# Optimization experiments

Hardware: AMD Instinct MI355X
Metric: run time of the kernel (lower is better)

## Reference

```python
import jax, jax.numpy as jnp
import numpy as np

N_NODES = 50000
N_EDGES = 600000
N_GRAPHS = 100
IN_DIM, HID, OUT = 128, 128, 64
K = 2  # DGL TAGConv default hop count


def setup_inputs() -> dict:
    key = jax.random.key(0)
    ks = jax.random.split(key, 8)
    x = jax.random.normal(ks[0], (N_NODES, IN_DIM), dtype=jnp.float32)
    src = jax.random.randint(ks[1], (N_EDGES,), 0, N_NODES)
    dst = jax.random.randint(ks[2], (N_EDGES,), 0, N_NODES)
    graph_id = jnp.sort(jax.random.randint(ks[3], (N_NODES,), 0, N_GRAPHS))
    # TAGConv lin: Linear(in_feats*(K+1), out_feats), stored as (in*(K+1), out)
    W1 = jax.random.normal(ks[4], (IN_DIM * (K + 1), HID), dtype=jnp.float32) / np.sqrt(IN_DIM * (K + 1))
    b1 = jnp.zeros((HID,), dtype=jnp.float32)
    W2 = jax.random.normal(ks[5], (HID * (K + 1), OUT), dtype=jnp.float32) / np.sqrt(HID * (K + 1))
    b2 = jnp.zeros((OUT,), dtype=jnp.float32)
    return {"x": x, "W1": W1, "b1": b1, "W2": W2, "b2": b2,
            "src": src, "dst": dst, "graph_id": graph_id}


def _tagconv(h, src, dst, norm, W, b):
    """DGL TAGConv: relu(concat_k (D^-1/2 A D^-1/2)^k h @ W + b), k=0..K."""
    feats = [h]
    cur = h
    for _ in range(K):
        cur = cur * norm[:, None]
        cur = jax.ops.segment_sum(cur[src], dst, num_segments=N_NODES)
        cur = cur * norm[:, None]
        feats.append(cur)
    out = jnp.concatenate(feats, axis=-1) @ W + b
    return jax.nn.relu(out)


def reference(x, W1, b1, W2, b2, src, dst, graph_id):
    # symmetric norm from in-degrees (clamped to 1), as in DGL TAGConv
    deg = jax.ops.segment_sum(jnp.ones_like(dst, dtype=x.dtype), dst, num_segments=N_NODES)
    norm = jnp.clip(deg, 1.0, None) ** -0.5
    h = _tagconv(x, src, dst, norm, W1, b1)
    h = _tagconv(h, src, dst, norm, W2, b2)
    # MaxPooling readout: per-graph max over nodes
    return jax.ops.segment_max(h, graph_id, num_segments=N_GRAPHS)
```

## Files before the change

kernel.cpp:

```cpp
#include <hip/hip_runtime.h>
#include <hip/hip_bf16.h>

#define N_NODES 50000
#define N_EDGES 600000
#define N_GRAPHS 100
#define M_PAD 50176

typedef __bf16 bf16_t;
typedef __attribute__((ext_vector_type(8))) __bf16 bf16x8;
typedef __attribute__((ext_vector_type(4))) __bf16 bf16x4;
typedef __attribute__((ext_vector_type(2))) __bf16 bf16x2;
typedef __attribute__((ext_vector_type(4))) float f32x4;

__global__ void degk(const int* __restrict__ dst, int* __restrict__ deg, int n) {
    int i = blockIdx.x * 256 + threadIdx.x;
    if (i < n) atomicAdd(&deg[dst[i]], 1);
}

__global__ __launch_bounds__(1024) void scan1(const int* __restrict__ deg,
                                              int* __restrict__ row_off,
                                              int* __restrict__ partial,
                                              float* __restrict__ norm, int n) {
    __shared__ int buf[1024];
    int i = blockIdx.x * 1024 + threadIdx.x;
    int v = (i < n) ? deg[i] : 0;
    buf[threadIdx.x] = v;
    __syncthreads();
    for (int off = 1; off < 1024; off <<= 1) {
        int t = (threadIdx.x >= off) ? buf[threadIdx.x - off] : 0;
        __syncthreads();
        buf[threadIdx.x] += t;
        __syncthreads();
    }
    if (i < n) {
        row_off[i + 1] = buf[threadIdx.x];
        float d = fmaxf((float)v, 1.0f);
        norm[i] = 1.0f / sqrtf(d);
    }
    if (threadIdx.x == 1023) partial[blockIdx.x] = buf[1023];
}

__global__ __launch_bounds__(256) void scan3(int* __restrict__ row_off,
                                             const int* __restrict__ partial, int n) {
    int i = blockIdx.x * 256 + threadIdx.x;
    int c = (blockIdx.x * 256) >> 10;
    __shared__ int pre;
    if (threadIdx.x < 64) {
        int v = (threadIdx.x < c) ? partial[threadIdx.x] : 0;
        for (int off = 32; off; off >>= 1) v += __shfl_down(v, off, 64);
        if (threadIdx.x == 0) pre = v;
    }
    __syncthreads();
    if (i == 0) row_off[0] = 0;
    if (i < n) row_off[i + 1] += pre;
}

#define NPRE 6250
#define NSC  ((N_EDGES + 255) / 256)
#define NPW  ((384 * 192 + 255) / 256)
__global__ __launch_bounds__(256) void midk(const float* __restrict__ x,
                                            const float* __restrict__ norm,
                                            bf16_t* __restrict__ xb, bf16_t* __restrict__ xs,
                                            const int* __restrict__ src, const int* __restrict__ dst,
                                            const int* __restrict__ row_off, int* __restrict__ cursor,
                                            int* __restrict__ csr_src,
                                            const float* __restrict__ W1, bf16_t* __restrict__ Wp1,
                                            const float* __restrict__ W2, bf16_t* __restrict__ Wp2) {
    int b = blockIdx.x;
    if (b < NPRE) {
        int i = b * 256 + threadIdx.x;
        int node = i >> 5, c4 = i & 31;
        float4 v = *(const float4*)(x + (size_t)node * 128 + c4 * 4);
        float nd = norm[node];
        bf16x4 ob, os;
        ob[0] = (bf16_t)v.x; ob[1] = (bf16_t)v.y; ob[2] = (bf16_t)v.z; ob[3] = (bf16_t)v.w;
        os[0] = (bf16_t)(v.x * nd); os[1] = (bf16_t)(v.y * nd);
        os[2] = (bf16_t)(v.z * nd); os[3] = (bf16_t)(v.w * nd);
        *(bf16x4*)(xb + (size_t)node * 128 + c4 * 4) = ob;
        *(bf16x4*)(xs + (size_t)node * 128 + c4 * 4) = os;
    } else if (b < NPRE + NSC) {
        int e = (b - NPRE) * 256 + threadIdx.x;
        if (e >= N_EDGES) return;
        int d = dst[e];
        int pos = atomicAdd(&cursor[d], 1);
        csr_src[row_off[d] + pos] = src[e];
    } else {
        int i = (b - NPRE - NSC) * 256 + threadIdx.x;
        const float* W; bf16_t* Wp; int N; int idx;
        if (i < 384 * 128)                 { W = W1; Wp = Wp1; N = 128; idx = i; }
        else if (i < 384 * 128 + 384 * 64) { W = W2; Wp = Wp2; N = 64;  idx = i - 384 * 128; }
        else return;
        int k = idx / N, n = idx - k * N;
        int kt = k >> 5, q = (k >> 3) & 3, j = k & 7;
        int nt = n >> 4, ln = n & 15;
        int lane = q * 16 + ln;
        Wp[(((size_t)kt * (N >> 4) + nt) * 64 + lane) * 8 + j] = (bf16_t)W[idx];
    }
}

template <bool SCALED>
__global__ __launch_bounds__(256) void spmm_bf16(const bf16_t* __restrict__ in,
                                                 bf16_t* __restrict__ out_c,
                                                 bf16_t* __restrict__ out_s,
                                                 const float* __restrict__ norm,
                                                 const int* __restrict__ row_off,
                                                 const int* __restrict__ csr_src, int n) {
    int tid = threadIdx.x;
    int sub = tid >> 4;
    int l   = tid & 15;
    int node = blockIdx.x * 16 + sub;
    if (node >= n) return;
    int e0 = row_off[node], e1 = row_off[node + 1];
    const bf16_t* col = in + l * 8;
    float acc[8] = {};
    int e = e0;
    for (; e + 8 <= e1; e += 8) {
        int s0 = csr_src[e + 0];
        int s1 = csr_src[e + 1];
        int s2 = csr_src[e + 2];
        int s3 = csr_src[e + 3];
        int s4 = csr_src[e + 4];
        int s5 = csr_src[e + 5];
        int s6 = csr_src[e + 6];
        int s7 = csr_src[e + 7];
        bf16x8 v0 = *(const bf16x8*)(col + (size_t)s0 * 128);
        bf16x8 v1 = *(const bf16x8*)(col + (size_t)s1 * 128);
        bf16x8 v2 = *(const bf16x8*)(col + (size_t)s2 * 128);
        bf16x8 v3 = *(const bf16x8*)(col + (size_t)s3 * 128);
        bf16x8 v4 = *(const bf16x8*)(col + (size_t)s4 * 128);
        bf16x8 v5 = *(const bf16x8*)(col + (size_t)s5 * 128);
        bf16x8 v6 = *(const bf16x8*)(col + (size_t)s6 * 128);
        bf16x8 v7 = *(const bf16x8*)(col + (size_t)s7 * 128);
#pragma unroll
        for (int j = 0; j < 8; j++)
            acc[j] += (((float)v0[j] + (float)v1[j]) + ((float)v2[j] + (float)v3[j]))
                    + (((float)v4[j] + (float)v5[j]) + ((float)v6[j] + (float)v7[j]));
    }
    if (e + 4 <= e1) {
        int s0 = csr_src[e + 0];
        int s1 = csr_src[e + 1];
        int s2 = csr_src[e + 2];
        int s3 = csr_src[e + 3];
        bf16x8 v0 = *(const bf16x8*)(col + (size_t)s0 * 128);
        bf16x8 v1 = *(const bf16x8*)(col + (size_t)s1 * 128);
        bf16x8 v2 = *(const bf16x8*)(col + (size_t)s2 * 128);
        bf16x8 v3 = *(const bf16x8*)(col + (size_t)s3 * 128);
#pragma unroll
        for (int j = 0; j < 8; j++)
            acc[j] += ((float)v0[j] + (float)v1[j]) + ((float)v2[j] + (float)v3[j]);
        e += 4;
    }
    for (; e < e1; e++) {
        int s = csr_src[e];
        bf16x8 v = *(const bf16x8*)(col + (size_t)s * 128);
#pragma unroll
        for (int j = 0; j < 8; j++) acc[j] += (float)v[j];
    }
    float nd = norm[node];
    bf16x8 oc, os;
#pragma unroll
    for (int j = 0; j < 8; j++) {
        float c = acc[j] * nd;
        oc[j] = (bf16_t)c;
        os[j] = (bf16_t)(c * nd);
    }
    *(bf16x8*)(out_c + (size_t)node * 128 + l * 8) = oc;
    if (SCALED) *(bf16x8*)(out_s + (size_t)node * 128 + l * 8) = os;
}

template <int NT, bool LAYER1>
__global__ __launch_bounds__(256) void gemm_mfma(const bf16_t* __restrict__ f0,
                                                 const bf16_t* __restrict__ f1,
                                                 const bf16_t* __restrict__ f2,
                                                 const bf16_t* __restrict__ Wp,
                                                 const float* __restrict__ bias,
                                                 const float* __restrict__ norm,
                                                 bf16_t* __restrict__ out_b,
                                                 bf16_t* __restrict__ out_s,
                                                 float* __restrict__ out_f, int M) {
    int wave = threadIdx.x >> 6;
    int lane = threadIdx.x & 63;
    int q = lane >> 4, ln = lane & 15;
    int row0 = blockIdx.x * 128 + wave * 32;

    f32x4 acc[2][NT] = {};
    const bf16_t* feats[3] = {f0, f1, f2};
    const bf16x8* Wf = (const bf16x8*)Wp;

#pragma unroll
    for (int kc = 0; kc < 12; kc++) {
        const bf16_t* A = feats[kc >> 2] + (size_t)(kc & 3) * 32 + q * 8;
        bf16x8 a0 = *(const bf16x8*)(A + (size_t)(row0 + ln) * 128);
        bf16x8 a1 = *(const bf16x8*)(A + (size_t)(row0 + 16 + ln) * 128);
        const bf16x8* Bp = Wf + (size_t)kc * NT * 64 + lane;
#pragma unroll
        for (int nt = 0; nt < NT; nt++) {
            bf16x8 b = Bp[nt * 64];
            acc[0][nt] = __builtin_amdgcn_mfma_f32_16x16x32_bf16(a0, b, acc[0][nt], 0, 0, 0);
            acc[1][nt] = __builtin_amdgcn_mfma_f32_16x16x32_bf16(a1, b, acc[1][nt], 0, 0, 0);
        }
    }

    float bv[NT];
#pragma unroll
    for (int nt = 0; nt < NT; nt++) bv[nt] = bias[nt * 16 + ln];

#pragma unroll
    for (int mt = 0; mt < 2; mt++) {
#pragma unroll
        for (int r = 0; r < 4; r++) {
            int row = row0 + mt * 16 + q * 4 + r;
            if (row >= M) continue;
            float nd = LAYER1 ? norm[row] : 0.f;
#pragma unroll
            for (int nt = 0; nt < NT; nt++) {
                int col = nt * 16 + ln;
                float val = fmaxf(acc[mt][nt][r] + bv[nt], 0.f);
                if (LAYER1) {
                    out_b[(size_t)row * 128 + col] = (bf16_t)val;
                    out_s[(size_t)row * 128 + col] = (bf16_t)(val * nd);
                } else {
                    out_f[(size_t)row * 64 + col] = val;
                }
            }
        }
    }
}

__global__ __launch_bounds__(256) void maxpool2(const float* __restrict__ hF,
                                                const int* __restrict__ gid,
                                                unsigned int* __restrict__ out, int n) {
    int wave = threadIdx.x >> 6;
    int lane = threadIdx.x & 63;
    int n0 = blockIdx.x * 256 + wave * 64;
    if (n0 >= n) return;
    int n1 = min(n0 + 64, n);
    int cur = gid[n0];
    float m = 0.f;
    int i = n0;
    for (; i + 4 <= n1; i += 4) {
        int g0 = gid[i + 0], g1 = gid[i + 1], g2 = gid[i + 2], g3 = gid[i + 3];
        float v0 = hF[(size_t)(i + 0) * 64 + lane];
        float v1 = hF[(size_t)(i + 1) * 64 + lane];
        float v2 = hF[(size_t)(i + 2) * 64 + lane];
        float v3 = hF[(size_t)(i + 3) * 64 + lane];
        if (g0 != cur) { atomicMax(&out[cur * 64 + lane], __float_as_uint(m)); cur = g0; m = v0; } else m = fmaxf(m, v0);
        if (g1 != cur) { atomicMax(&out[cur * 64 + lane], __float_as_uint(m)); cur = g1; m = v1; } else m = fmaxf(m, v1);
        if (g2 != cur) { atomicMax(&out[cur * 64 + lane], __float_as_uint(m)); cur = g2; m = v2; } else m = fmaxf(m, v2);
        if (g3 != cur) { atomicMax(&out[cur * 64 + lane], __float_as_uint(m)); cur = g3; m = v3; } else m = fmaxf(m, v3);
    }
    for (; i < n1; i++) {
        int g = gid[i];
        float v = hF[(size_t)i * 64 + lane];
        if (g != cur) { atomicMax(&out[cur * 64 + lane], __float_as_uint(m)); cur = g; m = v; }
        else m = fmaxf(m, v);
    }
    atomicMax(&out[cur * 64 + lane], __float_as_uint(m));
}

extern "C" void kernel_launch(void* const* d_in, const int* in_sizes, int n_in,
                              void* d_out, int out_size, void* d_ws, size_t ws_size,
                              hipStream_t stream) {
    const float* x  = (const float*)d_in[0];
    const float* W1 = (const float*)d_in[1];
    const float* b1 = (const float*)d_in[2];
    const float* W2 = (const float*)d_in[3];
    const float* b2 = (const float*)d_in[4];
    const int* src  = (const int*)d_in[5];
    const int* dst  = (const int*)d_in[6];
    const int* gid  = (const int*)d_in[7];
    float* out = (float*)d_out;

    char* ws = (char*)d_ws;
    size_t off = 0;
    auto take = [&](size_t bytes) {
        void* p = ws + off;
        off = (off + bytes + 255) & ~(size_t)255;
        return p;
    };
    int* deg     = (int*)take((size_t)N_NODES * 4);
    int* cursor  = (int*)take((size_t)N_NODES * 4);
    size_t zero_bytes = off;
    float* norm  = (float*)take((size_t)N_NODES * 4);
    int* row_off = (int*)take((size_t)(N_NODES + 1) * 4);
    int* partial = (int*)take(64 * 4);
    int* csr_src = (int*)take((size_t)N_EDGES * 4);
    bf16_t* Wp1  = (bf16_t*)take((size_t)384 * 128 * 2);
    bf16_t* Wp2  = (bf16_t*)take((size_t)384 * 64 * 2);
    bf16_t* B0 = (bf16_t*)take((size_t)M_PAD * 128 * 2);
    bf16_t* B1 = (bf16_t*)take((size_t)M_PAD * 128 * 2);
    bf16_t* B2 = (bf16_t*)take((size_t)M_PAD * 128 * 2);
    bf16_t* B3 = (bf16_t*)take((size_t)M_PAD * 128 * 2);
    bf16_t* B4 = (bf16_t*)take((size_t)M_PAD * 128 * 2);
    bf16_t* B5 = (bf16_t*)take((size_t)M_PAD * 128 * 2);
    (void)ws_size; (void)in_sizes; (void)n_in; (void)out_size;

    hipMemsetAsync(d_ws, 0, zero_bytes, stream);
    hipMemsetAsync(d_out, 0, (size_t)N_GRAPHS * 64 * 4, stream);

    degk<<<(N_EDGES + 255) / 256, 256, 0, stream>>>(dst, deg, N_EDGES);
    int nchunks = (N_NODES + 1023) / 1024;
    scan1<<<nchunks, 1024, 0, stream>>>(deg, row_off, partial, norm, N_NODES);
    scan3<<<(N_NODES + 255) / 256, 256, 0, stream>>>(row_off, partial, N_NODES);
    midk<<<NPRE + NSC + NPW, 256, 0, stream>>>(x, norm, B0, B1, src, dst, row_off, cursor,
                                               csr_src, W1, Wp1, W2, Wp2);

    int spmm_grid = (N_NODES + 15) / 16;
    int gemm_grid = M_PAD / 128;

    spmm_bf16<true><<<spmm_grid, 256, 0, stream>>>(B1, B2, B4, norm, row_off, csr_src, N_NODES);
    spmm_bf16<false><<<spmm_grid, 256, 0, stream>>>(B4, B3, nullptr, norm, row_off, csr_src, N_NODES);
    gemm_mfma<8, true><<<gemm_grid, 256, 0, stream>>>(B0, B2, B3, Wp1, b1, norm, B5, B1, nullptr, N_NODES);
    spmm_bf16<true><<<spmm_grid, 256, 0, stream>>>(B1, B2, B4, norm, row_off, csr_src, N_NODES);
    spmm_bf16<false><<<spmm_grid, 256, 0, stream>>>(B4, B3, nullptr, norm, row_off, csr_src, N_NODES);
    gemm_mfma<4, false><<<gemm_grid, 256, 0, stream>>>(B5, B2, B3, Wp2, b2, nullptr, nullptr, nullptr, (float*)B0, N_NODES);
    maxpool2<<<(N_NODES + 255) / 256, 256, 0, stream>>>((const float*)B0, gid, (unsigned int*)out, N_NODES);
}
```

Baseline: 310.2 us.

## Tile feature matrices into column slices mapped to XCDs for SpMM L2 locality

Feature buffers are stored as four 32-column slices, each laid out node-major. The SpMM grid is remapped so each pair of XCDs (by blockIdx & 7) gathers only one slice, shrinking each XCD's working set so it fits better in its private L2. Each node is now handled by 4 lanes instead of 16, so a wave covers 16 nodes. The CSR build also reuses the per-edge rank from the degree atomics instead of a second atomic cursor pass. The cost is an extra rank buffer and the assumption that the hardware dispatches blocks round-robin across XCDs.

```diff
diff --git a/kernel.cpp b/kernel.cpp
--- a/kernel.cpp
+++ b/kernel.cpp
@@ -5,6 +5,7 @@
 #define N_EDGES 600000
 #define N_GRAPHS 100
 #define M_PAD 50176
+#define TSLICE ((size_t)M_PAD * 32)
 
 typedef __bf16 bf16_t;
 typedef __attribute__((ext_vector_type(8))) __bf16 bf16x8;
@@ -12,9 +13,10 @@
 typedef __attribute__((ext_vector_type(2))) __bf16 bf16x2;
 typedef __attribute__((ext_vector_type(4))) float f32x4;
 
-__global__ void degk(const int* __restrict__ dst, int* __restrict__ deg, int n) {
+__global__ void degk(const int* __restrict__ dst, int* __restrict__ deg,
+                     int* __restrict__ rank, int n) {
     int i = blockIdx.x * 256 + threadIdx.x;
-    if (i < n) atomicAdd(&deg[dst[i]], 1);
+    if (i < n) rank[i] = atomicAdd(&deg[dst[i]], 1);
 }
 
 __global__ __launch_bounds__(1024) void scan1(const int* __restrict__ deg,
@@ -62,7 +64,8 @@
                                             const float* __restrict__ norm,
                                             bf16_t* __restrict__ xb, bf16_t* __restrict__ xs,
                                             const int* __restrict__ src, const int* __restrict__ dst,
-                                            const int* __restrict__ row_off, int* __restrict__ cursor,
+                                            const int* __restrict__ row_off,
+                                            const int* __restrict__ rank,
                                             int* __restrict__ csr_src,
                                             const float* __restrict__ W1, bf16_t* __restrict__ Wp1,
                                             const float* __restrict__ W2, bf16_t* __restrict__ Wp2) {
@@ -76,14 +79,14 @@
         ob[0] = (bf16_t)v.x; ob[1] = (bf16_t)v.y; ob[2] = (bf16_t)v.z; ob[3] = (bf16_t)v.w;
         os[0] = (bf16_t)(v.x * nd); os[1] = (bf16_t)(v.y * nd);
         os[2] = (bf16_t)(v.z * nd); os[3] = (bf16_t)(v.w * nd);
-        *(bf16x4*)(xb + (size_t)node * 128 + c4 * 4) = ob;
-        *(bf16x4*)(xs + (size_t)node * 128 + c4 * 4) = os;
+        size_t t = (size_t)(c4 >> 3) * TSLICE + (size_t)node * 32 + (c4 & 7) * 4;
+        *(bf16x4*)(xb + t) = ob;
+        *(bf16x4*)(xs + t) = os;
     } else if (b < NPRE + NSC) {
         int e = (b - NPRE) * 256 + threadIdx.x;
         if (e >= N_EDGES) return;
         int d = dst[e];
-        int pos = atomicAdd(&cursor[d], 1);
-        csr_src[row_off[d] + pos] = src[e];
+        csr_src[row_off[d] + rank[e]] = src[e];
     } else {
         int i = (b - NPRE - NSC) * 256 + threadIdx.x;
         const float* W; bf16_t* Wp; int N; int idx;
@@ -99,19 +102,22 @@
 }
 
 template <bool SCALED>
-__global__ __launch_bounds__(256) void spmm_bf16(const bf16_t* __restrict__ in,
-                                                 bf16_t* __restrict__ out_c,
-                                                 bf16_t* __restrict__ out_s,
-                                                 const float* __restrict__ norm,
-                                                 const int* __restrict__ row_off,
-                                                 const int* __restrict__ csr_src, int n) {
-    int tid = threadIdx.x;
-    int sub = tid >> 4;
-    int l   = tid & 15;
-    int node = blockIdx.x * 16 + sub;
+__global__ __launch_bounds__(256) void spmm_xcd(const bf16_t* __restrict__ in,
+                                                bf16_t* __restrict__ out_c,
+                                                bf16_t* __restrict__ out_s,
+                                                const float* __restrict__ norm,
+                                                const int* __restrict__ row_off,
+                                                const int* __restrict__ csr_src, int n) {
+    int bid  = blockIdx.x;
+    int xcd  = bid & 7;
+    int tile = xcd >> 1;
+    int sub  = bid >> 3;
+    int grp  = threadIdx.x >> 2;
+    int l    = threadIdx.x & 3;
+    int node = (sub * 2 + (xcd & 1)) * 64 + grp;
     if (node >= n) return;
     int e0 = row_off[node], e1 = row_off[node + 1];
-    const bf16_t* col = in + l * 8;
+    const bf16_t* base = in + (size_t)tile * TSLICE + l * 8;
     float acc[8] = {};
     int e = e0;
     for (; e + 8 <= e1; e += 8) {
@@ -123,14 +129,14 @@
         int s5 = csr_src[e + 5];
         int s6 = csr_src[e + 6];
         int s7 = csr_src[e + 7];
-        bf16x8 v0 = *(const bf16x8*)(col + (size_t)s0 * 128);
-        bf16x8 v1 = *(const bf16x8*)(col + (size_t)s1 * 128);
-        bf16x8 v2 = *(const bf16x8*)(col + (size_t)s2 * 128);
-        bf16x8 v3 = *(const bf16x8*)(col + (size_t)s3 * 128);
-        bf16x8 v4 = *(const bf16x8*)(col + (size_t)s4 * 128);
-        bf16x8 v5 = *(const bf16x8*)(col + (size_t)s5 * 128);
-        bf16x8 v6 = *(const bf16x8*)(col + (size_t)s6 * 128);
-        bf16x8 v7 = *(const bf16x8*)(col + (size_t)s7 * 128);
+        bf16x8 v0 = *(const bf16x8*)(base + (size_t)s0 * 32);
+        bf16x8 v1 = *(const bf16x8*)(base + (size_t)s1 * 32);
+        bf16x8 v2 = *(const bf16x8*)(base + (size_t)s2 * 32);
+        bf16x8 v3 = *(const bf16x8*)(base + (size_t)s3 * 32);
+        bf16x8 v4 = *(const bf16x8*)(base + (size_t)s4 * 32);
+        bf16x8 v5 = *(const bf16x8*)(base + (size_t)s5 * 32);
+        bf16x8 v6 = *(const bf16x8*)(base + (size_t)s6 * 32);
+        bf16x8 v7 = *(const bf16x8*)(base + (size_t)s7 * 32);
 #pragma unroll
         for (int j = 0; j < 8; j++)
             acc[j] += (((float)v0[j] + (float)v1[j]) + ((float)v2[j] + (float)v3[j]))
@@ -141,10 +147,10 @@
         int s1 = csr_src[e + 1];
         int s2 = csr_src[e + 2];
         int s3 = csr_src[e + 3];
-        bf16x8 v0 = *(const bf16x8*)(col + (size_t)s0 * 128);
-        bf16x8 v1 = *(const bf16x8*)(col + (size_t)s1 * 128);
-        bf16x8 v2 = *(const bf16x8*)(col + (size_t)s2 * 128);
-        bf16x8 v3 = *(const bf16x8*)(col + (size_t)s3 * 128);
+        bf16x8 v0 = *(const bf16x8*)(base + (size_t)s0 * 32);
+        bf16x8 v1 = *(const bf16x8*)(base + (size_t)s1 * 32);
+        bf16x8 v2 = *(const bf16x8*)(base + (size_t)s2 * 32);
+        bf16x8 v3 = *(const bf16x8*)(base + (size_t)s3 * 32);
 #pragma unroll
         for (int j = 0; j < 8; j++)
             acc[j] += ((float)v0[j] + (float)v1[j]) + ((float)v2[j] + (float)v3[j]);
@@ -152,7 +158,7 @@
     }
     for (; e < e1; e++) {
         int s = csr_src[e];
-        bf16x8 v = *(const bf16x8*)(col + (size_t)s * 128);
+        bf16x8 v = *(const bf16x8*)(base + (size_t)s * 32);
 #pragma unroll
         for (int j = 0; j < 8; j++) acc[j] += (float)v[j];
     }
@@ -164,8 +170,9 @@
         oc[j] = (bf16_t)c;
         os[j] = (bf16_t)(c * nd);
     }
-    *(bf16x8*)(out_c + (size_t)node * 128 + l * 8) = oc;
-    if (SCALED) *(bf16x8*)(out_s + (size_t)node * 128 + l * 8) = os;
+    size_t t = (size_t)tile * TSLICE + (size_t)node * 32 + l * 8;
+    *(bf16x8*)(out_c + t) = oc;
+    if (SCALED) *(bf16x8*)(out_s + t) = os;
 }
 
 template <int NT, bool LAYER1>
@@ -189,9 +196,9 @@
 
 #pragma unroll
     for (int kc = 0; kc < 12; kc++) {
-        const bf16_t* A = feats[kc >> 2] + (size_t)(kc & 3) * 32 + q * 8;
-        bf16x8 a0 = *(const bf16x8*)(A + (size_t)(row0 + ln) * 128);
-        bf16x8 a1 = *(const bf16x8*)(A + (size_t)(row0 + 16 + ln) * 128);
+        const bf16_t* A = feats[kc >> 2] + (size_t)(kc & 3) * TSLICE + q * 8;
+        bf16x8 a0 = *(const bf16x8*)(A + (size_t)(row0 + ln) * 32);
+        bf16x8 a1 = *(const bf16x8*)(A + (size_t)(row0 + 16 + ln) * 32);
         const bf16x8* Bp = Wf + (size_t)kc * NT * 64 + lane;
 #pragma unroll
         for (int nt = 0; nt < NT; nt++) {
@@ -214,13 +221,13 @@
             float nd = LAYER1 ? norm[row] : 0.f;
 #pragma unroll
             for (int nt = 0; nt < NT; nt++) {
-                int col = nt * 16 + ln;
                 float val = fmaxf(acc[mt][nt][r] + bv[nt], 0.f);
                 if (LAYER1) {
-                    out_b[(size_t)row * 128 + col] = (bf16_t)val;
-                    out_s[(size_t)row * 128 + col] = (bf16_t)(val * nd);
+                    size_t t = (size_t)(nt >> 1) * TSLICE + (size_t)row * 32 + (nt & 1) * 16 + ln;
+                    out_b[t] = (bf16_t)val;
+                    out_s[t] = (bf16_t)(val * nd);
                 } else {
-                    out_f[(size_t)row * 64 + col] = val;
+                    out_f[(size_t)row * 64 + nt * 16 + ln] = val;
                 }
             }
         }
@@ -279,11 +286,11 @@
         return p;
     };
     int* deg     = (int*)take((size_t)N_NODES * 4);
-    int* cursor  = (int*)take((size_t)N_NODES * 4);
     size_t zero_bytes = off;
     float* norm  = (float*)take((size_t)N_NODES * 4);
     int* row_off = (int*)take((size_t)(N_NODES + 1) * 4);
     int* partial = (int*)take(64 * 4);
+    int* rank    = (int*)take((size_t)N_EDGES * 4);
     int* csr_src = (int*)take((size_t)N_EDGES * 4);
     bf16_t* Wp1  = (bf16_t*)take((size_t)384 * 128 * 2);
     bf16_t* Wp2  = (bf16_t*)take((size_t)384 * 64 * 2);
@@ -298,21 +305,21 @@
     hipMemsetAsync(d_ws, 0, zero_bytes, stream);
     hipMemsetAsync(d_out, 0, (size_t)N_GRAPHS * 64 * 4, stream);
 
-    degk<<<(N_EDGES + 255) / 256, 256, 0, stream>>>(dst, deg, N_EDGES);
+    degk<<<(N_EDGES + 255) / 256, 256, 0, stream>>>(dst, deg, rank, N_EDGES);
     int nchunks = (N_NODES + 1023) / 1024;
     scan1<<<nchunks, 1024, 0, stream>>>(deg, row_off, partial, norm, N_NODES);
     scan3<<<(N_NODES + 255) / 256, 256, 0, stream>>>(row_off, partial, N_NODES);
-    midk<<<NPRE + NSC + NPW, 256, 0, stream>>>(x, norm, B0, B1, src, dst, row_off, cursor,
+    midk<<<NPRE + NSC + NPW, 256, 0, stream>>>(x, norm, B0, B1, src, dst, row_off, rank,
                                                csr_src, W1, Wp1, W2, Wp2);
 
-    int spmm_grid = (N_NODES + 15) / 16;
+    int spmm_grid = 8 * 391;
     int gemm_grid = M_PAD / 128;
 
-    spmm_bf16<true><<<spmm_grid, 256, 0, stream>>>(B1, B2, B4, norm, row_off, csr_src, N_NODES);
-    spmm_bf16<false><<<spmm_grid, 256, 0, stream>>>(B4, B3, nullptr, norm, row_off, csr_src, N_NODES);
+    spmm_xcd<true><<<spmm_grid, 256, 0, stream>>>(B1, B2, B4, norm, row_off, csr_src, N_NODES);
+    spmm_xcd<false><<<spmm_grid, 256, 0, stream>>>(B4, B3, nullptr, norm, row_off, csr_src, N_NODES);
     gemm_mfma<8, true><<<gemm_grid, 256, 0, stream>>>(B0, B2, B3, Wp1, b1, norm, B5, B1, nullptr, N_NODES);
-    spmm_bf16<true><<<spmm_grid, 256, 0, stream>>>(B1, B2, B4, norm, row_off, csr_src, N_NODES);
-    spmm_bf16<false><<<spmm_grid, 256, 0, stream>>>(B4, B3, nullptr, norm, row_off, csr_src, N_NODES);
+    spmm_xcd<true><<<spmm_grid, 256, 0, stream>>>(B1, B2, B4, norm, row_off, csr_src, N_NODES);
+    spmm_xcd<false><<<spmm_grid, 256, 0, stream>>>(B4, B3, nullptr, norm, row_off, csr_src, N_NODES);
     gemm_mfma<4, false><<<gemm_grid, 256, 0, stream>>>(B5, B2, B3, Wp2, b2, nullptr, nullptr, nullptr, (float*)B0, N_NODES);
     maxpool2<<<(N_NODES + 255) / 256, 256, 0, stream>>>((const float*)B0, gid, (unsigned int*)out, N_NODES);
 }
```

Result: faster. 281.8 us (-9.1%).
